# Optimization experiments

Measured on AMD Instinct MI355X. Metric: run time of the kernel, lower is better.

## Reference

```python
import jax, jax.numpy as jnp
import numpy as np

D_MODEL = 1024
N_HEADS = 16
HEAD_DIM = D_MODEL // N_HEADS
MAX_POS = 4096
ROPE_BASE = 10000.0
NEG_INF = -1e30


def _rope_cache(max_pos, head_dim, base):
    inv_freq = 1.0 / (base ** (np.arange(0, head_dim, 2, dtype=np.float32) / head_dim))
    t = np.arange(max_pos, dtype=np.float32)[:, None] * inv_freq[None, :]  # [P, D/2]
    cos = np.repeat(np.cos(t), 2, axis=-1)  # [P, D] (repeat_interleave)
    sin = np.repeat(np.sin(t), 2, axis=-1)
    return jnp.asarray(cos), jnp.asarray(sin)

COS_CACHE, SIN_CACHE = _rope_cache(MAX_POS, HEAD_DIM, ROPE_BASE)


def _rotate_half(x):
    # interleaved pairs: (x0,x1,x2,x3,...) -> (-x1,x0,-x3,x2,...)
    x1 = x[..., ::2]
    x2 = x[..., 1::2]
    return jnp.stack((-x2, x1), axis=-1).reshape(x.shape)


def setup_inputs() -> dict:
    key = jax.random.key(0)
    k0, k1, k2 = jax.random.split(key, 3)
    B, S = 4, 1024
    hidden_states = jax.random.normal(k0, (B, S, D_MODEL), dtype=jnp.float32)
    positions = jnp.arange(S, dtype=jnp.int64 if jax.config.jax_enable_x64 else jnp.int32)
    causal_mask = jnp.triu(jnp.ones((S, S), dtype=bool), k=1)  # True above diagonal -> masked
    # learned params (torch nn.Linear weight layout: [out, in], y = x @ W.T)
    Wqkv = jax.random.normal(k1, (3 * D_MODEL, D_MODEL), dtype=jnp.float32) * (D_MODEL ** -0.5)
    Wout = jax.random.normal(k2, (D_MODEL, D_MODEL), dtype=jnp.float32) * (D_MODEL ** -0.5)
    return {"hidden_states": hidden_states, "positions": positions,
            "causal_mask": causal_mask, "Wqkv": Wqkv, "Wout": Wout}


def reference(hidden_states, positions, causal_mask, Wqkv, Wout):
    B, S, D = hidden_states.shape
    qkv = hidden_states @ Wqkv.T                                   # [B,S,3D]
    qkv = qkv.reshape(B, S, 3, N_HEADS, HEAD_DIM)
    qkv = jnp.transpose(qkv, (2, 0, 3, 1, 4))                      # [3,B,H,S,Dh]
    q, k, v = qkv[0], qkv[1], qkv[2]
    # RoPE
    pos = jnp.clip(positions, 0, MAX_POS - 1)
    if pos.ndim == 1:
        pos = pos[None, :]
    cos = COS_CACHE[pos][:, None, :, :].astype(q.dtype)            # [B,1,S,Dh]
    sin = SIN_CACHE[pos][:, None, :, :].astype(q.dtype)
    q = q * cos + _rotate_half(q) * sin
    k = k * cos + _rotate_half(k) * sin
    # SDPA with causal bias (F.scaled_dot_product_attention default scaling)
    scale = HEAD_DIM ** -0.5
    scores = jnp.einsum('bhqd,bhkd->bhqk', q, k) * scale           # [B,H,S,S]
    scores = jnp.where(causal_mask[None, None, :, :], NEG_INF, scores)
    probs = jax.nn.softmax(scores, axis=-1)
    attn = jnp.einsum('bhqk,bhkd->bhqd', probs, v)                 # [B,H,S,Dh]
    attn = jnp.transpose(attn, (0, 2, 1, 3)).reshape(B, S, D)
    return attn @ Wout.T
```

## Files before the change

kernel.cpp:

```cpp
#include <hip/hip_runtime.h>

typedef __attribute__((ext_vector_type(8))) short short8;
typedef __attribute__((ext_vector_type(4))) float f32x4;

#define MFMA(a, b, c) __builtin_amdgcn_mfma_f32_16x16x32_bf16((a), (b), (c), 0, 0, 0)

#define S_LEN 1024
#define DM 1024
#define NHEADS 16
#define HD 64
#define NBH 64
#define MAXPOS 4096

__device__ __forceinline__ ushort f2bf(float f) {
    unsigned u = __builtin_bit_cast(unsigned, f);
    u += 0x7fffu + ((u >> 16) & 1u);
    return (ushort)(u >> 16);
}
__device__ __forceinline__ float bf2f(ushort h) {
    return __builtin_bit_cast(float, (unsigned)h << 16);
}

__device__ __forceinline__ void gload16(const ushort* g, ushort* l) {
    __builtin_amdgcn_global_load_lds(
        (const __attribute__((address_space(1))) unsigned int*)g,
        (__attribute__((address_space(3))) unsigned int*)l, 16, 0, 0);
}

__global__ __launch_bounds__(256) void k_cvt3(const float4* __restrict__ hs,
                                              const float4* __restrict__ wqkv,
                                              const float4* __restrict__ wout,
                                              ushort4* __restrict__ hsB,
                                              ushort4* __restrict__ wqkvB,
                                              ushort4* __restrict__ woutB,
                                              float* __restrict__ tab) {
    int id = blockIdx.x * 256 + threadIdx.x;
    if (id < 2097152) {
        const float4* src;
        ushort4* dst;
        int off;
        if (id < 1048576)      { src = hs;   dst = hsB;   off = id; }
        else if (id < 1835008) { src = wqkv; dst = wqkvB; off = id - 1048576; }
        else                   { src = wout; dst = woutB; off = id - 1835008; }
        float4 v = src[off];
        ushort4 o;
        o.x = f2bf(v.x); o.y = f2bf(v.y); o.z = f2bf(v.z); o.w = f2bf(v.w);
        dst[off] = o;
    } else {
        int t = id - 2097152;
        int p = t >> 5, i = t & 31;
        float inv = powf(10000.f, -(float)(2 * i) / 64.f);
        float th = (float)p * inv;
        float s, c;
        sincosf(th, &s, &c);
        tab[2 * t] = c;
        tab[2 * t + 1] = s;
    }
}

template <int MODE>
__global__ __launch_bounds__(256, 3) void k_gemm(
    const ushort* __restrict__ A, const ushort* __restrict__ BT,
    float* __restrict__ Cf,
    const int* __restrict__ pos, const float* __restrict__ tab,
    ushort* __restrict__ Qh, ushort* __restrict__ Kh, ushort* __restrict__ Vt,
    int M, int N, int K, int nbx) {
    __shared__ __align__(16) ushort SH[3 * 8192];
    const int tid = threadIdx.x;
    const int lane = tid & 63, wave = tid >> 6;
    const int wr = wave >> 1, wc = wave & 1;
    const int l15 = lane & 15, lhi = lane >> 4;
    const int nby = gridDim.x / nbx;
    const int xcd = blockIdx.x & 7, idx = blockIdx.x >> 3;
    const int Creg = nbx >> 1, Rreg = nby >> 2;
    const int by = (xcd >> 1) * Rreg + idx / Creg;
    const int bx = (xcd & 1) * Creg + idx % Creg;
    const int m0 = by << 7, n0 = bx << 7;

    const int srow = tid >> 2;
    const int scol = (((tid >> 2) & 3) ^ ((tid >> 4) & 3) ^ (tid & 3)) << 3;
    const int fcol = ((lhi ^ ((l15 & 3) ^ ((l15 >> 2) & 3)))) << 3;

    f32x4 acc[4][4];
#pragma unroll
    for (int i = 0; i < 4; ++i)
#pragma unroll
        for (int j = 0; j < 4; ++j) acc[i][j] = 0;

#define STAGE(bs, kb)                                                           \
    do {                                                                        \
        ushort* bb = SH + (bs) * 8192;                                          \
        gload16(&A[(size_t)(m0 + srow) * K + (kb) + scol], bb + tid * 8);       \
        gload16(&A[(size_t)(m0 + 64 + srow) * K + (kb) + scol],                 \
                bb + 2048 + tid * 8);                                           \
        gload16(&BT[(size_t)(n0 + srow) * K + (kb) + scol],                     \
                bb + 4096 + tid * 8);                                           \
        gload16(&BT[(size_t)(n0 + 64 + srow) * K + (kb) + scol],                \
                bb + 6144 + tid * 8);                                           \
    } while (0)

    const int nk = K >> 5;
    STAGE(0, 0);
    STAGE(1, 32);
    int bi = 0;
    for (int t = 0; t < nk; ++t) {
        if (t + 1 < nk) {
            asm volatile("s_waitcnt vmcnt(4)" ::: "memory");
        } else {
            asm volatile("s_waitcnt vmcnt(0)" ::: "memory");
        }
        __builtin_amdgcn_s_barrier();
        __builtin_amdgcn_sched_barrier(0);
        if (t + 2 < nk) {
            int bs = bi + 2;
            if (bs >= 3) bs -= 3;
            STAGE(bs, (t + 2) << 5);
        }
        const ushort* bufA = SH + bi * 8192;
        const ushort* bufB = bufA + 4096;
        short8 a[4], b[4];
#pragma unroll
        for (int fm = 0; fm < 4; ++fm)
            a[fm] = *(const short8*)&bufA[(wr * 64 + fm * 16 + l15) * 32 + fcol];
#pragma unroll
        for (int fn = 0; fn < 4; ++fn)
            b[fn] = *(const short8*)&bufB[(wc * 64 + fn * 16 + l15) * 32 + fcol];
#pragma unroll
        for (int fm = 0; fm < 4; ++fm)
#pragma unroll
            for (int fn = 0; fn < 4; ++fn)
                acc[fm][fn] = MFMA(a[fm], b[fn], acc[fm][fn]);
        bi = (bi == 2) ? 0 : bi + 1;
    }
#undef STAGE
    __syncthreads();

    if (MODE == 0) {
#pragma unroll
        for (int fm = 0; fm < 4; ++fm)
#pragma unroll
            for (int fn = 0; fn < 4; ++fn)
#pragma unroll
                for (int i = 0; i < 4; ++i) {
                    int row = m0 + wr * 64 + fm * 16 + lhi * 4 + i;
                    int col = n0 + wc * 64 + fn * 16 + l15;
                    Cf[(size_t)row * N + col] = acc[fm][fn][i];
                }
    } else {
        const int sec = n0 >> 10;
        if (sec < 2) {
            ushort* dstb = sec == 0 ? Qh : Kh;
            const float qs = sec == 0 ? 0.125f : 1.0f;
#pragma unroll
            for (int fm = 0; fm < 4; ++fm)
#pragma unroll
                for (int i = 0; i < 4; ++i) {
                    const int row = m0 + wr * 64 + fm * 16 + lhi * 4 + i;
                    const int b = row >> 10, s = row & 1023;
                    int p = pos[s];
                    p = p < 0 ? 0 : (p > MAXPOS - 1 ? MAXPOS - 1 : p);
#pragma unroll
                    for (int fn = 0; fn < 4; ++fn) {
                        const int col = n0 + wc * 64 + fn * 16 + l15;
                        const int cw = col & 1023;
                        const int h = cw >> 6, d = cw & 63;
                        const float c  = tab[((size_t)p * 32 + (d >> 1)) * 2];
                        const float sn = tab[((size_t)p * 32 + (d >> 1)) * 2 + 1];
                        const float v = acc[fm][fn][i];
                        const float pr = __shfl_xor(v, 1);
                        const float o = (d & 1) ? (v * c + pr * sn) : (v * c - pr * sn);
                        dstb[((size_t)((b * 16 + h) * 1024 + s)) * 64 + d] = f2bf(o * qs);
                    }
                }
        } else {
            ushort (*T)[132] = (ushort(*)[132]) & SH[0];
#pragma unroll
            for (int fm = 0; fm < 4; ++fm)
#pragma unroll
                for (int fn = 0; fn < 4; ++fn)
#pragma unroll
                    for (int i = 0; i < 4; ++i)
                        T[wr * 64 + fm * 16 + lhi * 4 + i][wc * 64 + fn * 16 + l15] =
                            f2bf(acc[fm][fn][i]);
            __syncthreads();
            const int b = m0 >> 10, s0 = m0 & 1023;
            const int dd = tid & 127, scg = tid >> 7;
            const int hv = ((n0 & 1023) >> 6) + (dd >> 6);
            const int d = dd & 63;
            ushort* dst = Vt + ((size_t)(b * 16 + hv) * 64 + d) * S_LEN + s0;
#pragma unroll
            for (int j = 0; j < 8; ++j) {
                const int ch = scg * 8 + j;
                __align__(16) ushort tmp[8];
#pragma unroll
                for (int e = 0; e < 8; ++e) tmp[e] = T[ch * 8 + e][dd];
                *(uint4*)&dst[ch * 8] = *(uint4*)tmp;
            }
        }
    }
}

__global__ __launch_bounds__(256, 3) void k_attn(const ushort* __restrict__ Qh,
                                                 const ushort* __restrict__ Kh,
                                                 const ushort* __restrict__ Vt,
                                                 ushort* __restrict__ attnB) {
    __shared__ __align__(16) ushort Ks[2][64][64];
    __shared__ __align__(16) ushort Vs[2][64][64];
    __shared__ __align__(16) ushort P[4][16][72];
    const int bh = blockIdx.x;
    const int g  = blockIdx.y;
    const int gA = g, gB = 15 - g;
    const int nkb = gB + 1;
    const int tid = threadIdx.x;
    const int wave = tid >> 6, lane = tid & 63;
    const int l15 = lane & 15, lhi = lane >> 4;
    const int b = bh >> 4, h = bh & 15;
    const ushort* Qp = Qh + (size_t)bh * S_LEN * 64;
    const ushort* Kp = Kh + (size_t)bh * S_LEN * 64;
    const ushort* Vp = Vt + (size_t)bh * 64 * S_LEN;
    const int qbA = (gA << 6) + (wave << 4);
    const int qbB = (gB << 6) + (wave << 4);
    const int qrowbA = qbA + lhi * 4;
    const int qrowbB = qbB + lhi * 4;

    const int U0 = tid, U1 = tid + 256;
    const int r0 = U0 >> 3, o0 = ((U0 & 7) ^ (r0 & 7)) << 3;
    const int r1 = U1 >> 3, o1 = ((U1 & 7) ^ (r1 & 7)) << 3;
    ushort* KsF = &Ks[0][0][0];
    ushort* VsF = &Vs[0][0][0];

    short8 aQA0 = *(const short8*)&Qp[(size_t)(qbA + l15) * 64 + lhi * 8];
    short8 aQA1 = *(const short8*)&Qp[(size_t)(qbA + l15) * 64 + 32 + lhi * 8];
    short8 aQB0 = *(const short8*)&Qp[(size_t)(qbB + l15) * 64 + lhi * 8];
    short8 aQB1 = *(const short8*)&Qp[(size_t)(qbB + l15) * 64 + 32 + lhi * 8];

    short8 ones;
#pragma unroll
    for (int j = 0; j < 8; ++j) ones[j] = (short)0x3F80;

    f32x4 OA0{}, OA1{}, OA2{}, OA3{}, ssumA{};
    f32x4 OB0{}, OB1{}, OB2{}, OB3{}, ssumB{};

    gload16(&Kp[(size_t)r0 * 64 + o0], KsF + U0 * 8);
    gload16(&Kp[(size_t)r1 * 64 + o1], KsF + U1 * 8);
    gload16(&Vp[(size_t)r0 * S_LEN + o0], VsF + U0 * 8);
    gload16(&Vp[(size_t)r1 * S_LEN + o1], VsF + U1 * 8);
    __syncthreads();

#define LDSK(s, kk) (*(const short8*)(KsF + (cur << 12) + ((((s) << 4) + l15) << 6) + \
                                      ((((kk) * 4 + lhi) ^ (l15 & 7)) << 3)))
#define LDSV(n, kk) (*(const short8*)(VsF + (cur << 12) + ((((n) << 4) + l15) << 6) + \
                                      ((((kk) * 4 + lhi) ^ (l15 & 7)) << 3)))
#define EXPST(SV, SUB)                                                         \
    _Pragma("unroll") for (int i = 0; i < 4; ++i) {                            \
        P[wave][lhi * 4 + i][(SUB) * 16 + l15] = f2bf(__expf(SV[i] - 8.f));    \
    }
#define EXPSTM(SV, SUB, QROWB)                                                 \
    _Pragma("unroll") for (int i = 0; i < 4; ++i) {                            \
        float v = SV[i];                                                       \
        if (k0 + (SUB) * 16 + l15 > (QROWB) + i) v = -1e30f;                   \
        P[wave][lhi * 4 + i][(SUB) * 16 + l15] = f2bf(__expf(v - 8.f));        \
    }

    int cur = 0;
    for (int kb = 0; kb < nkb; ++kb) {
        const int k0 = kb << 6;
        if (kb + 1 < nkb) {
            const int kn = k0 + 64;
            const int bo = (cur ^ 1) << 12;
            gload16(&Kp[(size_t)(kn + r0) * 64 + o0], KsF + bo + U0 * 8);
            gload16(&Kp[(size_t)(kn + r1) * 64 + o1], KsF + bo + U1 * 8);
            gload16(&Vp[(size_t)r0 * S_LEN + kn + o0], VsF + bo + U0 * 8);
            gload16(&Vp[(size_t)r1 * S_LEN + kn + o1], VsF + bo + U1 * 8);
        }

        if (kb <= gA) {
            __builtin_amdgcn_s_setprio(1);
            f32x4 s0{}, s1{}, s2{}, s3{};
            s0 = MFMA(aQA0, LDSK(0, 0), s0); s0 = MFMA(aQA1, LDSK(0, 1), s0);
            s1 = MFMA(aQA0, LDSK(1, 0), s1); s1 = MFMA(aQA1, LDSK(1, 1), s1);
            s2 = MFMA(aQA0, LDSK(2, 0), s2); s2 = MFMA(aQA1, LDSK(2, 1), s2);
            s3 = MFMA(aQA0, LDSK(3, 0), s3); s3 = MFMA(aQA1, LDSK(3, 1), s3);
            __builtin_amdgcn_s_setprio(0);
            if (kb == gA) {
                EXPSTM(s0, 0, qrowbA) EXPSTM(s1, 1, qrowbA)
                EXPSTM(s2, 2, qrowbA) EXPSTM(s3, 3, qrowbA)
            } else {
                EXPST(s0, 0) EXPST(s1, 1) EXPST(s2, 2) EXPST(s3, 3)
            }
            short8 aP0 = *(const short8*)&P[wave][l15][lhi * 8];
            short8 aP1 = *(const short8*)&P[wave][l15][32 + lhi * 8];
            __builtin_amdgcn_s_setprio(1);
            ssumA = MFMA(aP0, ones, ssumA); ssumA = MFMA(aP1, ones, ssumA);
            OA0 = MFMA(aP0, LDSV(0, 0), OA0); OA0 = MFMA(aP1, LDSV(0, 1), OA0);
            OA1 = MFMA(aP0, LDSV(1, 0), OA1); OA1 = MFMA(aP1, LDSV(1, 1), OA1);
            OA2 = MFMA(aP0, LDSV(2, 0), OA2); OA2 = MFMA(aP1, LDSV(2, 1), OA2);
            OA3 = MFMA(aP0, LDSV(3, 0), OA3); OA3 = MFMA(aP1, LDSV(3, 1), OA3);
            __builtin_amdgcn_s_setprio(0);
        }

        {
            __builtin_amdgcn_s_setprio(1);
            f32x4 s0{}, s1{}, s2{}, s3{};
            s0 = MFMA(aQB0, LDSK(0, 0), s0); s0 = MFMA(aQB1, LDSK(0, 1), s0);
            s1 = MFMA(aQB0, LDSK(1, 0), s1); s1 = MFMA(aQB1, LDSK(1, 1), s1);
            s2 = MFMA(aQB0, LDSK(2, 0), s2); s2 = MFMA(aQB1, LDSK(2, 1), s2);
            s3 = MFMA(aQB0, LDSK(3, 0), s3); s3 = MFMA(aQB1, LDSK(3, 1), s3);
            __builtin_amdgcn_s_setprio(0);
            if (kb == gB) {
                EXPSTM(s0, 0, qrowbB) EXPSTM(s1, 1, qrowbB)
                EXPSTM(s2, 2, qrowbB) EXPSTM(s3, 3, qrowbB)
            } else {
                EXPST(s0, 0) EXPST(s1, 1) EXPST(s2, 2) EXPST(s3, 3)
            }
            short8 aP0 = *(const short8*)&P[wave][l15][lhi * 8];
            short8 aP1 = *(const short8*)&P[wave][l15][32 + lhi * 8];
            __builtin_amdgcn_s_setprio(1);
            ssumB = MFMA(aP0, ones, ssumB); ssumB = MFMA(aP1, ones, ssumB);
            OB0 = MFMA(aP0, LDSV(0, 0), OB0); OB0 = MFMA(aP1, LDSV(0, 1), OB0);
            OB1 = MFMA(aP0, LDSV(1, 0), OB1); OB1 = MFMA(aP1, LDSV(1, 1), OB1);
            OB2 = MFMA(aP0, LDSV(2, 0), OB2); OB2 = MFMA(aP1, LDSV(2, 1), OB2);
            OB3 = MFMA(aP0, LDSV(3, 0), OB3); OB3 = MFMA(aP1, LDSV(3, 1), OB3);
            __builtin_amdgcn_s_setprio(0);
        }

        __syncthreads();
        cur ^= 1;
    }
#undef LDSK
#undef LDSV
#undef EXPST
#undef EXPSTM

#define WOUT(OV, N, QB, INV)                                                   \
    _Pragma("unroll") for (int i = 0; i < 4; ++i) {                            \
        int row = (QB) + lhi * 4 + i;                                          \
        attnB[((size_t)(b * S_LEN + row)) * DM + h * 64 + (N) * 16 + l15] =    \
            f2bf(OV[i] * INV[i]);                                              \
    }
    {
        f32x4 invA, invB;
#pragma unroll
        for (int i = 0; i < 4; ++i) {
            invA[i] = 1.f / ssumA[i];
            invB[i] = 1.f / ssumB[i];
        }
        WOUT(OA0, 0, qbA, invA) WOUT(OA1, 1, qbA, invA)
        WOUT(OA2, 2, qbA, invA) WOUT(OA3, 3, qbA, invA)
        WOUT(OB0, 0, qbB, invB) WOUT(OB1, 1, qbB, invB)
        WOUT(OB2, 2, qbB, invB) WOUT(OB3, 3, qbB, invB)
    }
#undef WOUT
}

extern "C" void kernel_launch(void* const* d_in, const int* in_sizes, int n_in,
                              void* d_out, int out_size, void* d_ws, size_t ws_size,
                              hipStream_t stream) {
    (void)in_sizes; (void)n_in; (void)out_size; (void)ws_size;
    const float* hs   = (const float*)d_in[0];
    const int*   pos  = (const int*)d_in[1];
    const float* Wqkv = (const float*)d_in[3];
    const float* Wout = (const float*)d_in[4];
    float* out = (float*)d_out;

    char* ws = (char*)d_ws;
    size_t off = 0;
    ushort* hsB   = (ushort*)(ws + off); off += (size_t)4096 * 1024 * 2;
    ushort* WqkvB = (ushort*)(ws + off); off += (size_t)3072 * 1024 * 2;
    ushort* WoutB = (ushort*)(ws + off); off += (size_t)1024 * 1024 * 2;
    ushort* Qh    = (ushort*)(ws + off); off += (size_t)NBH * 1024 * 64 * 2;
    ushort* Kh    = (ushort*)(ws + off); off += (size_t)NBH * 1024 * 64 * 2;
    ushort* Vt    = (ushort*)(ws + off); off += (size_t)NBH * 64 * 1024 * 2;
    ushort* attnB = (ushort*)(ws + off); off += (size_t)4096 * 1024 * 2;
    float*  tab   = (float*)(ws + off);  off += (size_t)4096 * 32 * 2 * 4;

    k_cvt3<<<8704, 256, 0, stream>>>((const float4*)hs, (const float4*)Wqkv,
                                     (const float4*)Wout, (ushort4*)hsB,
                                     (ushort4*)WqkvB, (ushort4*)WoutB, tab);

    k_gemm<1><<<768, 256, 0, stream>>>(hsB, WqkvB, nullptr, pos, tab,
                                       Qh, Kh, Vt, 4096, 3072, 1024, 24);

    k_attn<<<dim3(64, 8), 256, 0, stream>>>(Qh, Kh, Vt, attnB);

    k_gemm<0><<<256, 256, 0, stream>>>(attnB, WoutB, out, nullptr, nullptr,
                                       nullptr, nullptr, nullptr, 4096, 1024, 1024, 8);
}
```

Measured before the change: 93.14 us.

## Use 256x256 tile, 8-wave QKV GEMM with 4-stage pipelined LDS loads

Replaces the 128x128 QKV projection GEMM with a dedicated 256x256-tile kernel that uses 512 threads and a 4-buffer global-to-LDS pipeline. It splits each k-step into two MFMA phases with explicit barriers, waitcnts and setprio, and keeps the fused RoPE and V-transpose epilogues. The goal is more operand reuse per LDS byte and better overlap of loads with MFMA. The cost is a grid of only 192 blocks on a 256-CU part, which leaves many CUs idle, plus heavier register and LDS use.

After: 98.98 us. +6.3%, slower.

```diff
diff --git a/kernel.cpp b/kernel.cpp
--- a/kernel.cpp
+++ b/kernel.cpp
@@ -58,13 +58,159 @@
     }
 }
 
-template <int MODE>
-__global__ __launch_bounds__(256, 3) void k_gemm(
+__global__ __launch_bounds__(512, 2) void k_gemm256(
     const ushort* __restrict__ A, const ushort* __restrict__ BT,
-    float* __restrict__ Cf,
     const int* __restrict__ pos, const float* __restrict__ tab,
-    ushort* __restrict__ Qh, ushort* __restrict__ Kh, ushort* __restrict__ Vt,
-    int M, int N, int K, int nbx) {
+    ushort* __restrict__ Qh, ushort* __restrict__ Kh, ushort* __restrict__ Vt) {
+    __shared__ __align__(16) ushort SH[4 * 16384];
+    const int K = 1024;
+    const int tid = threadIdx.x;
+    const int lane = tid & 63, wave = tid >> 6;
+    const int wr = wave >> 2, wc = wave & 3;
+    const int l15 = lane & 15, lhi = lane >> 4;
+    const int bx = blockIdx.x % 12, by = blockIdx.x / 12;
+    const int m0 = by << 8, n0 = bx << 8;
+    const int fcol = ((lhi ^ ((l15 & 3) ^ ((l15 >> 2) & 3)))) << 3;
+
+    f32x4 acc[8][4];
+#pragma unroll
+    for (int i = 0; i < 8; ++i)
+#pragma unroll
+        for (int j = 0; j < 4; ++j) acc[i][j] = 0;
+
+#define STAGE(bs, kb)                                                           \
+    do {                                                                        \
+        ushort* bb = SH + (bs) * 16384;                                         \
+        _Pragma("unroll") for (int k = 0; k < 4; ++k) {                         \
+            const int u = tid + k * 512;                                        \
+            const int r = (u & 1023) >> 2;                                      \
+            const int sc = ((u & 3) ^ (r & 3) ^ ((r >> 2) & 3)) << 3;           \
+            const ushort* src = (k < 2)                                         \
+                ? &A[(size_t)(m0 + r) * K + (kb) + sc]                          \
+                : &BT[(size_t)(n0 + r) * K + (kb) + sc];                        \
+            gload16(src, bb + u * 8);                                           \
+        }                                                                       \
+    } while (0)
+
+    const int nk = K >> 5;
+    STAGE(0, 0);
+    STAGE(1, 32);
+    STAGE(2, 64);
+    int bi = 0;
+    for (int t = 0; t < nk; ++t) {
+        if (t + 2 < nk) {
+            asm volatile("s_waitcnt vmcnt(8)" ::: "memory");
+        } else if (t + 1 < nk) {
+            asm volatile("s_waitcnt vmcnt(4)" ::: "memory");
+        } else {
+            asm volatile("s_waitcnt vmcnt(0)" ::: "memory");
+        }
+        __builtin_amdgcn_s_barrier();
+        __builtin_amdgcn_sched_barrier(0);
+        const ushort* buf = SH + bi * 16384;
+
+        short8 a0[4], b[4];
+#pragma unroll
+        for (int nf = 0; nf < 4; ++nf)
+            b[nf] = *(const short8*)&buf[8192 + (wc * 64 + nf * 16 + l15) * 32 + fcol];
+#pragma unroll
+        for (int mf = 0; mf < 4; ++mf)
+            a0[mf] = *(const short8*)&buf[(wr * 128 + mf * 16 + l15) * 32 + fcol];
+        if (t + 3 < nk) STAGE((bi + 3) & 3, (t + 3) << 5);
+        __builtin_amdgcn_s_barrier();
+        asm volatile("s_waitcnt lgkmcnt(0)" ::: "memory");
+        __builtin_amdgcn_sched_barrier(0);
+        __builtin_amdgcn_s_setprio(1);
+#pragma unroll
+        for (int mf = 0; mf < 4; ++mf)
+#pragma unroll
+            for (int nf = 0; nf < 4; ++nf)
+                acc[mf][nf] = MFMA(a0[mf], b[nf], acc[mf][nf]);
+        __builtin_amdgcn_s_setprio(0);
+        __builtin_amdgcn_s_barrier();
+        __builtin_amdgcn_sched_barrier(0);
+
+        short8 a1[4];
+#pragma unroll
+        for (int mf = 0; mf < 4; ++mf)
+            a1[mf] = *(const short8*)&buf[(wr * 128 + (mf + 4) * 16 + l15) * 32 + fcol];
+        __builtin_amdgcn_s_barrier();
+        asm volatile("s_waitcnt lgkmcnt(0)" ::: "memory");
+        __builtin_amdgcn_sched_barrier(0);
+        __builtin_amdgcn_s_setprio(1);
+#pragma unroll
+        for (int mf = 0; mf < 4; ++mf)
+#pragma unroll
+            for (int nf = 0; nf < 4; ++nf)
+                acc[mf + 4][nf] = MFMA(a1[mf], b[nf], acc[mf + 4][nf]);
+        __builtin_amdgcn_s_setprio(0);
+        bi = (bi + 1) & 3;
+    }
+#undef STAGE
+    __syncthreads();
+
+    const int sec = n0 >> 10;
+    if (sec < 2) {
+        ushort* dstb = sec == 0 ? Qh : Kh;
+        const float qs = sec == 0 ? 0.125f : 1.0f;
+#pragma unroll
+        for (int mf = 0; mf < 8; ++mf)
+#pragma unroll
+            for (int i = 0; i < 4; ++i) {
+                const int row = m0 + wr * 128 + mf * 16 + lhi * 4 + i;
+                const int b = row >> 10, s = row & 1023;
+                int p = pos[s];
+                p = p < 0 ? 0 : (p > MAXPOS - 1 ? MAXPOS - 1 : p);
+#pragma unroll
+                for (int nf = 0; nf < 4; ++nf) {
+                    const int col = n0 + wc * 64 + nf * 16 + l15;
+                    const int cw = col & 1023;
+                    const int h = cw >> 6, d = cw & 63;
+                    const float c  = tab[((size_t)p * 32 + (d >> 1)) * 2];
+                    const float sn = tab[((size_t)p * 32 + (d >> 1)) * 2 + 1];
+                    const float v = acc[mf][nf][i];
+                    const float pr = __shfl_xor(v, 1);
+                    const float o = (d & 1) ? (v * c + pr * sn) : (v * c - pr * sn);
+                    dstb[((size_t)((b * 16 + h) * 1024 + s)) * 64 + d] = f2bf(o * qs);
+                }
+            }
+    } else {
+        ushort (*T)[264] = (ushort(*)[264]) & SH[0];
+        const int bb = m0 >> 10;
+        const int dd = tid & 255, sg = tid >> 8;
+        const int hv = ((n0 & 1023) >> 6) + (dd >> 6);
+        const int d = dd & 63;
+#pragma unroll
+        for (int h = 0; h < 2; ++h) {
+            if (wr == h) {
+#pragma unroll
+                for (int mf = 0; mf < 8; ++mf)
+#pragma unroll
+                    for (int nf = 0; nf < 4; ++nf)
+#pragma unroll
+                        for (int i = 0; i < 4; ++i)
+                            T[mf * 16 + lhi * 4 + i][wc * 64 + nf * 16 + l15] =
+                                f2bf(acc[mf][nf][i]);
+            }
+            __syncthreads();
+            const int s0 = (m0 & 1023) + h * 128;
+            ushort* dst = Vt + ((size_t)(bb * 16 + hv) * 64 + d) * S_LEN + s0;
+#pragma unroll
+            for (int j = 0; j < 8; ++j) {
+                const int ch = sg * 8 + j;
+                __align__(16) ushort tmp[8];
+#pragma unroll
+                for (int e = 0; e < 8; ++e) tmp[e] = T[ch * 8 + e][dd];
+                *(uint4*)&dst[ch * 8] = *(uint4*)tmp;
+            }
+            __syncthreads();
+        }
+    }
+}
+
+__global__ __launch_bounds__(256, 3) void k_gemm_out(
+    const ushort* __restrict__ A, const ushort* __restrict__ BT,
+    float* __restrict__ Cf, int M, int N, int K, int nbx) {
     __shared__ __align__(16) ushort SH[3 * 8192];
     const int tid = threadIdx.x;
     const int lane = tid & 63, wave = tid >> 6;
@@ -133,71 +279,17 @@
         bi = (bi == 2) ? 0 : bi + 1;
     }
 #undef STAGE
-    __syncthreads();
-
-    if (MODE == 0) {
-#pragma unroll
-        for (int fm = 0; fm < 4; ++fm)
-#pragma unroll
-            for (int fn = 0; fn < 4; ++fn)
-#pragma unroll
-                for (int i = 0; i < 4; ++i) {
-                    int row = m0 + wr * 64 + fm * 16 + lhi * 4 + i;
-                    int col = n0 + wc * 64 + fn * 16 + l15;
-                    Cf[(size_t)row * N + col] = acc[fm][fn][i];
-                }
-    } else {
-        const int sec = n0 >> 10;
-        if (sec < 2) {
-            ushort* dstb = sec == 0 ? Qh : Kh;
-            const float qs = sec == 0 ? 0.125f : 1.0f;
-#pragma unroll
-            for (int fm = 0; fm < 4; ++fm)
-#pragma unroll
-                for (int i = 0; i < 4; ++i) {
-                    const int row = m0 + wr * 64 + fm * 16 + lhi * 4 + i;
-                    const int b = row >> 10, s = row & 1023;
-                    int p = pos[s];
-                    p = p < 0 ? 0 : (p > MAXPOS - 1 ? MAXPOS - 1 : p);
-#pragma unroll
-                    for (int fn = 0; fn < 4; ++fn) {
-                        const int col = n0 + wc * 64 + fn * 16 + l15;
-                        const int cw = col & 1023;
-                        const int h = cw >> 6, d = cw & 63;
-                        const float c  = tab[((size_t)p * 32 + (d >> 1)) * 2];
-                        const float sn = tab[((size_t)p * 32 + (d >> 1)) * 2 + 1];
-                        const float v = acc[fm][fn][i];
-                        const float pr = __shfl_xor(v, 1);
-                        const float o = (d & 1) ? (v * c + pr * sn) : (v * c - pr * sn);
-                        dstb[((size_t)((b * 16 + h) * 1024 + s)) * 64 + d] = f2bf(o * qs);
-                    }
-                }
-        } else {
-            ushort (*T)[132] = (ushort(*)[132]) & SH[0];
-#pragma unroll
-            for (int fm = 0; fm < 4; ++fm)
-#pragma unroll
-                for (int fn = 0; fn < 4; ++fn)
-#pragma unroll
-                    for (int i = 0; i < 4; ++i)
-                        T[wr * 64 + fm * 16 + lhi * 4 + i][wc * 64 + fn * 16 + l15] =
-                            f2bf(acc[fm][fn][i]);
-            __syncthreads();
-            const int b = m0 >> 10, s0 = m0 & 1023;
-            const int dd = tid & 127, scg = tid >> 7;
-            const int hv = ((n0 & 1023) >> 6) + (dd >> 6);
-            const int d = dd & 63;
-            ushort* dst = Vt + ((size_t)(b * 16 + hv) * 64 + d) * S_LEN + s0;
-#pragma unroll
-            for (int j = 0; j < 8; ++j) {
-                const int ch = scg * 8 + j;
-                __align__(16) ushort tmp[8];
-#pragma unroll
-                for (int e = 0; e < 8; ++e) tmp[e] = T[ch * 8 + e][dd];
-                *(uint4*)&dst[ch * 8] = *(uint4*)tmp;
-            }
-        }
-    }
+
+#pragma unroll
+    for (int fm = 0; fm < 4; ++fm)
+#pragma unroll
+        for (int fn = 0; fn < 4; ++fn)
+#pragma unroll
+            for (int i = 0; i < 4; ++i) {
+                int row = m0 + wr * 64 + fm * 16 + lhi * 4 + i;
+                int col = n0 + wc * 64 + fn * 16 + l15;
+                Cf[(size_t)row * N + col] = acc[fm][fn][i];
+            }
 }
 
 __global__ __launch_bounds__(256, 3) void k_attn(const ushort* __restrict__ Qh,
@@ -378,11 +470,9 @@
                                      (const float4*)Wout, (ushort4*)hsB,
                                      (ushort4*)WqkvB, (ushort4*)WoutB, tab);
 
-    k_gemm<1><<<768, 256, 0, stream>>>(hsB, WqkvB, nullptr, pos, tab,
-                                       Qh, Kh, Vt, 4096, 3072, 1024, 24);
+    k_gemm256<<<192, 512, 0, stream>>>(hsB, WqkvB, pos, tab, Qh, Kh, Vt);
 
     k_attn<<<dim3(64, 8), 256, 0, stream>>>(Qh, Kh, Vt, attnB);
 
-    k_gemm<0><<<256, 256, 0, stream>>>(attnB, WoutB, out, nullptr, nullptr,
-                                       nullptr, nullptr, nullptr, 4096, 1024, 1024, 8);
-}
+    k_gemm_out<<<256, 256, 0, stream>>>(attnB, WoutB, out, 4096, 1024, 1024, 8);
+}
```
